# Kernel optimization log

Measured on AMD Instinct MI355X. Metric: run time of the kernel, lower is better.

## Reference

```python
import jax, jax.numpy as jnp
import numpy as np

D_CAT = 4096   # number of multinomial categories (input_dim)
HID = 256      # hidden_dim
B = 4096       # batch_size (eta is a (B, D_CAT-1) parameter)
INIT = 1e-3
LOG2PI = float(np.log(2.0 * np.pi))


def _helmert_basis(d):
    """Orthonormal ILR balance basis, shape (d-1, d): rows sum to 0, Psi @ Psi.T = I."""
    i = np.arange(1, d, dtype=np.float64)
    scale = np.sqrt(i / (i + 1.0))
    Psi = np.zeros((d - 1, d), dtype=np.float64)
    tri = np.tril(np.ones((d - 1, d - 1), dtype=np.float64))
    Psi[:, : d - 1] = tri * (scale / i)[:, None]
    Psi[np.arange(d - 1), np.arange(1, d)] = -scale
    return Psi.astype(np.float32)


def setup_inputs() -> dict:
    key = jax.random.key(0)
    k1, k2, k3, k4 = jax.random.split(key, 4)
    n = D_CAT - 1
    x = jax.random.randint(k1, (B, D_CAT), 0, 20).astype(jnp.float32)  # count data
    Psi = jnp.asarray(_helmert_basis(D_CAT))                            # (n, D)
    enc_W = jax.random.normal(k2, (HID, n), dtype=jnp.float32) * INIT   # encoder Linear weight
    dec_W = jax.random.normal(k3, (n, HID), dtype=jnp.float32) * INIT   # decoder Linear weight
    variational_logvars = jnp.zeros((HID,), jnp.float32)
    log_sigma_sq = jnp.float32(0.01)
    eta = jax.random.normal(k4, (B, n), dtype=jnp.float32) * INIT       # learned eta parameter
    return dict(x=x, Psi=Psi, enc_W=enc_W, dec_W=dec_W,
                variational_logvars=variational_logvars,
                log_sigma_sq=log_sigma_sq, eta=eta)


def reference(x, Psi, enc_W, dec_W, variational_logvars, log_sigma_sq, eta):
    # --- ILR transform of imputed counts: clr(log(x+1)) @ Psi^T ---
    logp = jnp.log(x + 1.0)                                   # imputer: x + 1
    clr = logp - logp.mean(-1, keepdims=True)                 # (B, D)
    hx = clr @ Psi.T                                          # (B, n)
    z_mean = hx @ enc_W.T                                     # (B, k)
    mu = z_mean @ dec_W.T                                     # (B, n)

    # --- MultivariateNormalFactorIdentity log_prob via Woodbury / det lemma ---
    # Sigma = var * I_n + W diag(Dv) W^T,  W = dec_W (n, k)
    Dv = jnp.exp(variational_logvars)                         # (k,)
    var = jnp.exp(log_sigma_sq)                               # scalar
    n = dec_W.shape[0]
    WtW = dec_W.T @ dec_W                                     # (k, k)
    M = jnp.diag(1.0 / Dv) + WtW / var                        # capacitance matrix (k, k)
    d = eta - mu                                              # (B, n)
    dW = d @ dec_W                                            # (B, k)
    sol = jnp.linalg.solve(M, dW.T).T                         # (B, k)
    quad = jnp.sum(d * d, -1) / var - jnp.sum(dW * sol, -1) / (var * var)
    _, logdetM = jnp.linalg.slogdet(M)
    logdet_sigma = n * log_sigma_sq + jnp.sum(variational_logvars) + logdetM
    logit_loss = jnp.mean(-0.5 * (n * LOG2PI + logdet_sigma + quad))

    # --- standard-normal prior on z_mean ---
    prior_loss = jnp.mean(-0.5 * z_mean * z_mean - 0.5 * LOG2PI)

    # --- Multinomial log-likelihood with logits = ilr_inv(eta) = eta @ Psi ---
    logits = eta @ Psi                                        # (B, D)
    logsm = jax.nn.log_softmax(logits, -1)
    ntot = x.sum(-1)
    mult = (jax.lax.lgamma(ntot + 1.0)
            - jnp.sum(jax.lax.lgamma(x + 1.0), -1)
            + jnp.sum(x * logsm, -1))
    mult_loss = jnp.mean(mult)

    return -(mult_loss + logit_loss + prior_loss)
```

## Files before the change

kernel.cpp:

```cpp
#include <hip/hip_runtime.h>
#include <math.h>

static constexpr int DC  = 4096;
static constexpr int NM1 = 4095;
static constexpr int HID = 256;
static constexpr int BB  = 4096;
static constexpr double LOG2PI_D = 1.8378770664093454835;

typedef __attribute__((ext_vector_type(8))) __bf16 bf16x8;
typedef __attribute__((ext_vector_type(4))) __bf16 bf16x4;
typedef __attribute__((ext_vector_type(2))) __bf16 bf16x2;
typedef __attribute__((ext_vector_type(4))) float  f32x4;

__device__ __forceinline__ void async16(const __bf16* g, __bf16* l) {
    __builtin_amdgcn_global_load_lds(
        (const __attribute__((address_space(1))) void*)g,
        (__attribute__((address_space(3))) void*)l, 16, 0, 0);
}

__global__ __launch_bounds__(256) void k_pre(
    const float* __restrict__ decW, const float* __restrict__ Psi,
    const float* __restrict__ lv, const float* __restrict__ lss,
    __bf16* __restrict__ decWT, float* __restrict__ av, float* __restrict__ bv,
    float* __restrict__ Dv, float* __restrict__ scal)
{
    __shared__ float tp[32][33];
    const int t = threadIdx.x;
    const int blk = blockIdx.x;
    if (blk < 1024) {
        int bx = blk & 7, by = blk >> 3;
        int tx = t & 31, ty = t >> 5;
        int r0 = by * 32, c0 = bx * 32;
        #pragma unroll
        for (int i = 0; i < 4; i++) {
            int r = r0 + ty + i * 8, c = c0 + tx;
            tp[ty + i * 8][tx] = (r < NM1 && c < HID) ? decW[(size_t)r * HID + c] : 0.f;
        }
        __syncthreads();
        #pragma unroll
        for (int i = 0; i < 4; i++) {
            int c = c0 + ty + i * 8, r = r0 + tx;
            decWT[(size_t)c * DC + r] = (__bf16)tp[tx][ty + i * 8];
        }
    } else if (blk < 1040) {
        int r = (blk - 1024) * 256 + t;
        if (r < NM1) {
            av[r] = Psi[(size_t)r * DC];
            bv[r] = -Psi[(size_t)r * DC + r + 1];
        } else { av[r] = 0.f; bv[r] = 0.f; }
    } else {
        float v = lv[t];
        Dv[t] = expf(v);
        for (int o = 32; o > 0; o >>= 1) v += __shfl_down(v, o);
        __shared__ float red[4];
        if ((t & 63) == 0) red[t >> 6] = v;
        __syncthreads();
        if (t == 0) {
            scal[0] = expf(lss[0]);
            scal[1] = red[0] + red[1] + red[2] + red[3];
        }
    }
}

__global__ __launch_bounds__(256) void k_mega(
    const float* __restrict__ x, const float* __restrict__ eta,
    const float* __restrict__ encW, const __bf16* __restrict__ decWT,
    const float* __restrict__ av, const float* __restrict__ bv,
    float* __restrict__ multv, float* __restrict__ eta2,
    __bf16* __restrict__ clrB, __bf16* __restrict__ etaB,
    __bf16* __restrict__ encPsiB, float* __restrict__ WtW)
{
    __shared__ float smemf[2392];
    const int t = threadIdx.x;
    const int blk = blockIdx.x;
    const int lane = t & 63, w = t >> 6;

    if (blk >= 64 + HID) {
        __bf16* es    = (__bf16*)smemf;
        float* red    = smemf + 2048;
        float* wsumE  = smemf + 2064;
        float* wsumX  = smemf + 2068;
        float* firstX = smemf + 2072;
        float* lutL   = smemf + 2328;
        float* lutG   = smemf + 2360;
        const int b = blk - (64 + HID);
        const int j0 = t * 16;

        const float4* xrow = (const float4*)(x + (size_t)b * DC + j0);
        float4 xq[4];
        #pragma unroll
        for (int i = 0; i < 4; i++) xq[i] = xrow[i];

        const float* erow = eta + (size_t)b * NM1;
        float ee[16];
        #pragma unroll
        for (int i = 0; i < 16; i++) { int j = i * 256 + t; ee[i] = (j < NM1) ? erow[j] : 0.f; }

        float avc[16], bvc[16];
        #pragma unroll
        for (int i = 0; i < 16; i += 4) {
            float4 a4 = *(const float4*)(av + j0 + i);
            avc[i] = a4.x; avc[i + 1] = a4.y; avc[i + 2] = a4.z; avc[i + 3] = a4.w;
            float4 b4 = *(const float4*)(bv + j0 + i);
            bvc[i] = b4.x; bvc[i + 1] = b4.y; bvc[i + 2] = b4.z; bvc[i + 3] = b4.w;
        }

        if (t < 32) { float f = (float)t + 1.f; lutL[t] = logf(f); lutG[t] = lgammaf(f); }
        __syncthreads();

        float xv[16], lvv[16];
        #pragma unroll
        for (int i = 0; i < 4; i++) {
            xv[i * 4 + 0] = xq[i].x; xv[i * 4 + 1] = xq[i].y;
            xv[i * 4 + 2] = xq[i].z; xv[i * 4 + 3] = xq[i].w;
        }
        float s = 0.f, slg = 0.f, slp = 0.f;
        #pragma unroll
        for (int i = 0; i < 16; i++) {
            float vf = xv[i];
            int iv = (int)vf;
            float l, g;
            if (vf == (float)iv && iv >= 0 && iv < 32) { l = lutL[iv]; g = lutG[iv]; }
            else { l = logf(vf + 1.f); g = lgammaf(vf + 1.f); }
            lvv[i] = l;
            s += vf; slg += g; slp += l;
        }
        float e2 = 0.f;
        #pragma unroll
        for (int i = 0; i < 16; i++) {
            float e = ee[i];
            e2 += e * e;
            es[i * 256 + t] = (__bf16)e;
        }
        firstX[t] = xv[0];
        for (int o = 32; o > 0; o >>= 1) {
            s += __shfl_down(s, o); slg += __shfl_down(slg, o);
            slp += __shfl_down(slp, o); e2 += __shfl_down(e2, o);
        }
        if (lane == 0) { red[w] = s; red[4 + w] = slg; red[8 + w] = slp; red[12 + w] = e2; }
        __syncthreads();

        const float ntotv  = red[0] + red[1] + red[2] + red[3];
        const float sumlgv = red[4] + red[5] + red[6] + red[7];
        const float m = (red[8] + red[9] + red[10] + red[11]) * (1.f / DC);

        bf16x8 e0 = *(const bf16x8*)(es + j0);
        bf16x8 e1 = *(const bf16x8*)(es + j0 + 8);
        *(bf16x8*)(etaB + (size_t)b * DC + j0)     = e0;
        *(bf16x8*)(etaB + (size_t)b * DC + j0 + 8) = e1;
        float ev[16];
        #pragma unroll
        for (int i = 0; i < 8; i++) { ev[i] = (float)e0[i]; ev[i + 8] = (float)e1[i]; }

        bf16x8 c0, c1;
        #pragma unroll
        for (int i = 0; i < 8; i++) {
            c0[i] = (__bf16)(lvv[i] - m);
            c1[i] = (__bf16)(lvv[i + 8] - m);
        }
        *(bf16x8*)(clrB + (size_t)b * DC + j0)     = c0;
        *(bf16x8*)(clrB + (size_t)b * DC + j0 + 8) = c1;

        float localE = 0.f, localX = 0.f;
        #pragma unroll
        for (int i = 0; i < 16; i++) { localE += ev[i] * avc[i]; localX += xv[i]; }
        float incE = localE, incX = localX;
        #pragma unroll
        for (int o = 1; o < 64; o <<= 1) {
            float vE = __shfl_up(incE, o), vX = __shfl_up(incX, o);
            if (lane >= o) { incE += vE; incX += vX; }
        }
        if (lane == 63) { wsumE[w] = incE; wsumX[w] = incX; }
        float eprev = (t > 0) ? (float)es[j0 - 1] : 0.f;
        float bprev = (t > 0) ? bv[j0 - 1] : 0.f;
        float xnl   = (t < 255) ? firstX[t + 1] : 0.f;
        __syncthreads();

        float woffE = 0.f, woffX = 0.f;
        for (int i = 0; i < w; i++) { woffE += wsumE[i]; woffX += wsumX[i]; }
        const float U = wsumE[0] + wsumE[1] + wsumE[2] + wsumE[3];
        float runE = woffE + incE - localE;
        float Xrun = woffX + incX - localX;

        float se = 0.f, sx = 0.f;
        #pragma unroll
        for (int i = 0; i < 16; i++) {
            float Tj = U - runE;
            runE += ev[i] * avc[i];
            float pw = (i == 0) ? eprev * bprev : ev[i - 1] * bvc[i - 1];
            float l = Tj - pw;
            se += expf(l);
            Xrun += xv[i];
            float xn = (i < 15) ? xv[i + 1] : xnl;
            sx += ev[i] * (avc[i] * Xrun - bvc[i] * xn);
        }
        for (int o = 32; o > 0; o >>= 1) {
            se += __shfl_down(se, o); sx += __shfl_down(sx, o);
        }
        if (lane == 0) { red[0 + w] = se; red[4 + w] = sx; }
        __syncthreads();
        if (t == 0) {
            float S1t = red[0] + red[1] + red[2] + red[3];
            float S2t = red[4] + red[5] + red[6] + red[7];
            float e2t = red[12] + red[13] + red[14] + red[15];
            double mult = (double)lgammaf(ntotv + 1.f) - (double)sumlgv
                        + (double)S2t - (double)ntotv * (double)logf(S1t);
            multv[b] = (float)mult;
            eta2[b]  = e2t;
        }
    } else if (blk >= 64) {
        __bf16* es   = (__bf16*)smemf;
        float* wsumE = smemf + 2048;
        const int h = blk - 64;
        const float* erow = encW + (size_t)h * NM1;
        float ee[16];
        #pragma unroll
        for (int i = 0; i < 16; i++) { int j = i * 256 + t; ee[i] = (j < NM1) ? erow[j] : 0.f; }
        const int j0 = t * 16;
        float avc[16], bvc[16];
        #pragma unroll
        for (int i = 0; i < 16; i += 4) {
            float4 a4 = *(const float4*)(av + j0 + i);
            avc[i] = a4.x; avc[i + 1] = a4.y; avc[i + 2] = a4.z; avc[i + 3] = a4.w;
            float4 b4 = *(const float4*)(bv + j0 + i);
            bvc[i] = b4.x; bvc[i + 1] = b4.y; bvc[i + 2] = b4.z; bvc[i + 3] = b4.w;
        }
        #pragma unroll
        for (int i = 0; i < 16; i++) es[i * 256 + t] = (__bf16)ee[i];
        __syncthreads();
        float ev[16];
        {
            bf16x8 ea = *(const bf16x8*)(es + j0), eb8 = *(const bf16x8*)(es + j0 + 8);
            #pragma unroll
            for (int i = 0; i < 8; i++) { ev[i] = (float)ea[i]; ev[i + 8] = (float)eb8[i]; }
        }
        float localE = 0.f;
        #pragma unroll
        for (int i = 0; i < 16; i++) localE += ev[i] * avc[i];
        float incE = localE;
        #pragma unroll
        for (int o = 1; o < 64; o <<= 1) { float vE = __shfl_up(incE, o); if (lane >= o) incE += vE; }
        if (lane == 63) wsumE[w] = incE;
        float eprev = (t > 0) ? (float)es[j0 - 1] : 0.f;
        float bprev = (t > 0) ? bv[j0 - 1] : 0.f;
        __syncthreads();
        float woffE = 0.f;
        for (int i = 0; i < w; i++) woffE += wsumE[i];
        const float U = wsumE[0] + wsumE[1] + wsumE[2] + wsumE[3];
        float runE = woffE + incE - localE;
        bf16x8 o0, o1;
        #pragma unroll
        for (int i = 0; i < 16; i++) {
            float Tj = U - runE;
            runE += ev[i] * avc[i];
            float pw = (i == 0) ? eprev * bprev : ev[i - 1] * bvc[i - 1];
            float l = Tj - pw;
            if (i < 8) o0[i] = (__bf16)l; else o1[i - 8] = (__bf16)l;
        }
        *(bf16x8*)(encPsiB + (size_t)h * DC + j0)     = o0;
        *(bf16x8*)(encPsiB + (size_t)h * DC + j0 + 8) = o1;
    } else {
        __bf16* As = (__bf16*)smemf;
        __bf16* Bs = (__bf16*)(smemf + 1024);
        const int w2 = blk;
        const int mn = w2 & 15, sl = w2 >> 4;
        const int m0 = (mn >> 2) * 64, n0 = (mn & 3) * 64, kb = sl * 1024;
        const int ln = lane & 15, q = lane >> 4;
        const int wm = w >> 1, wn = w & 1;
        f32x4 acc[2][2] = {};
        for (int k0 = kb; k0 < kb + 1024; k0 += 32) {
            async16(decWT + (size_t)(m0 + (t >> 2)) * DC + k0 + (t & 3) * 8, As + t * 8);
            async16(decWT + (size_t)(n0 + (t >> 2)) * DC + k0 + (t & 3) * 8, Bs + t * 8);
            __syncthreads();
            bf16x8 af[2], bfr[2];
            #pragma unroll
            for (int i = 0; i < 2; i++) {
                af[i]  = *(const bf16x8*)(As + (wm * 32 + i * 16 + ln) * 32 + q * 8);
                bfr[i] = *(const bf16x8*)(Bs + (wn * 32 + i * 16 + ln) * 32 + q * 8);
            }
            #pragma unroll
            for (int mi = 0; mi < 2; mi++)
                #pragma unroll
                for (int ni = 0; ni < 2; ni++)
                    acc[mi][ni] = __builtin_amdgcn_mfma_f32_16x16x32_bf16(af[mi], bfr[ni], acc[mi][ni], 0, 0, 0);
            __syncthreads();
        }
        #pragma unroll
        for (int mi = 0; mi < 2; mi++)
            #pragma unroll
            for (int rr = 0; rr < 4; rr++) {
                int m = m0 + wm * 32 + mi * 16 + q * 4 + rr;
                #pragma unroll
                for (int ni = 0; ni < 2; ni++)
                    atomicAdd(&WtW[(size_t)m * HID + n0 + wn * 32 + ni * 16 + ln], acc[mi][ni][rr]);
            }
    }
}

__global__ __launch_bounds__(256) void k_combo2(
    const __bf16* __restrict__ clrB, const __bf16* __restrict__ etaB,
    const __bf16* __restrict__ encPsiB, const __bf16* __restrict__ decWT,
    float* __restrict__ part,
    const float* __restrict__ WtW, const float* __restrict__ Dv,
    const float* __restrict__ scal, __bf16* __restrict__ WtWB,
    __bf16* __restrict__ MinvB, float* __restrict__ scal_out)
{
    __shared__ __bf16 As[64 * 64];
    __shared__ __bf16 Bs[256 * 64];
    const int tid = threadIdx.x;
    const int w = tid >> 6, lane = tid & 63;
    const int ln = lane & 15, q = lane >> 4;
    const int wm = w >> 1, wn = w & 1;
    const int bid = blockIdx.x;

    if (bid >= 16) {
        const int idx = bid - 16;
        const int g = idx >> 8, r = idx & 255, sl = r >> 6, mt = r & 63;
        const __bf16* A  = g ? etaB  : clrB;
        const __bf16* Bt = g ? decWT : encPsiB;
        float* C = part + ((size_t)(g * 4 + sl) << 20);
        const int m0 = mt * 64, kb = sl * 1024;
        f32x4 acc[2][8] = {};
        for (int k0 = kb; k0 < kb + 1024; k0 += 64) {
            #pragma unroll
            for (int j = 0; j < 2; j++) {
                int c = j * 256 + tid;
                int row = c >> 3, ch = c & 7;
                async16(A + (size_t)(m0 + row) * DC + k0 + (ch ^ (row & 7)) * 8, As + c * 8);
            }
            #pragma unroll
            for (int j = 0; j < 8; j++) {
                int c = j * 256 + tid;
                int row = c >> 3, ch = c & 7;
                async16(Bt + (size_t)row * DC + k0 + (ch ^ (row & 7)) * 8, Bs + c * 8);
            }
            __syncthreads();
            #pragma unroll
            for (int jj = 0; jj < 2; jj++) {
                bf16x8 af[2], bfr[8];
                #pragma unroll
                for (int i = 0; i < 2; i++) {
                    int arow = wm * 32 + i * 16 + ln;
                    af[i]  = *(const bf16x8*)(As + arow * 64 + ((jj * 4 + q) ^ (arow & 7)) * 8);
                }
                #pragma unroll
                for (int i = 0; i < 8; i++) {
                    int brow = wn * 128 + i * 16 + ln;
                    bfr[i] = *(const bf16x8*)(Bs + brow * 64 + ((jj * 4 + q) ^ (brow & 7)) * 8);
                }
                #pragma unroll
                for (int mi = 0; mi < 2; mi++)
                    #pragma unroll
                    for (int ni = 0; ni < 8; ni++)
                        acc[mi][ni] = __builtin_amdgcn_mfma_f32_16x16x32_bf16(af[mi], bfr[ni], acc[mi][ni], 0, 0, 0);
            }
            __syncthreads();
        }
        #pragma unroll
        for (int mi = 0; mi < 2; mi++)
            #pragma unroll
            for (int rr = 0; rr < 4; rr++) {
                int m = m0 + wm * 32 + mi * 16 + q * 4 + rr;
                #pragma unroll
                for (int ni = 0; ni < 8; ni++) {
                    int n = wn * 128 + ni * 16 + ln;
                    C[(size_t)m * HID + n] = acc[mi][ni][rr];
                }
            }
    } else {
        __shared__ float dvs[HID];
        __shared__ float redc[8];
        const int w2 = bid;
        const int m0 = (w2 >> 2) * 64, n0 = (w2 & 3) * 64;
        dvs[tid] = Dv[tid];
        __syncthreads();
        const float rv = 1.f / scal[0];
        f32x4 acc[2][2] = {};
        for (int k0 = 0; k0 < HID; k0 += 32) {
            {
                int row = tid >> 2, kc = tid & 3;
                const float* srcA = WtW + (size_t)(m0 + row) * HID + k0 + kc * 8;
                const float* srcB = WtW + (size_t)(n0 + row) * HID + k0 + kc * 8;
                float sA = dvs[m0 + row] * rv;
                bf16x8 a8, b8;
                #pragma unroll
                for (int u = 0; u < 8; u++) {
                    a8[u] = (__bf16)(srcA[u] * sA);
                    b8[u] = (__bf16)(srcB[u] * dvs[k0 + kc * 8 + u] * rv);
                }
                *(bf16x8*)(As + tid * 8) = a8;
                *(bf16x8*)(Bs + tid * 8) = b8;
            }
            __syncthreads();
            bf16x8 af[2], bfr[2];
            #pragma unroll
            for (int i = 0; i < 2; i++) {
                af[i]  = *(const bf16x8*)(As + (wm * 32 + i * 16 + ln) * 32 + q * 8);
                bfr[i] = *(const bf16x8*)(Bs + (wn * 32 + i * 16 + ln) * 32 + q * 8);
            }
            #pragma unroll
            for (int mi = 0; mi < 2; mi++)
                #pragma unroll
                for (int ni = 0; ni < 2; ni++)
                    acc[mi][ni] = __builtin_amdgcn_mfma_f32_16x16x32_bf16(af[mi], bfr[ni], acc[mi][ni], 0, 0, 0);
            __syncthreads();
        }
        float t1p = 0.f, t2p = 0.f;
        #pragma unroll
        for (int mi = 0; mi < 2; mi++)
            #pragma unroll
            for (int rr = 0; rr < 4; rr++) {
                int m = m0 + wm * 32 + mi * 16 + q * 4 + rr;
                #pragma unroll
                for (int ni = 0; ni < 2; ni++) {
                    int n = n0 + wn * 32 + ni * 16 + ln;
                    float wmn = WtW[(size_t)m * HID + n];
                    float Bmn = dvs[m] * wmn * rv;
                    float Bnm = dvs[n] * wmn * rv;
                    float mv = (((m == n) ? 1.f : 0.f) - Bmn + acc[mi][ni][rr]) * dvs[n];
                    MinvB[(size_t)m * HID + n] = (__bf16)mv;
                    WtWB[(size_t)m * HID + n] = (__bf16)wmn;
                    t2p += Bmn * Bnm;
                    if (m == n) t1p += Bmn;
                }
            }
        for (int o = 32; o > 0; o >>= 1) { t1p += __shfl_down(t1p, o); t2p += __shfl_down(t2p, o); }
        if (lane == 0) { redc[w] = t1p; redc[4 + w] = t2p; }
        __syncthreads();
        if (tid == 0) {
            atomicAdd(&scal_out[2], redc[0] + redc[1] + redc[2] + redc[3]);
            atomicAdd(&scal_out[3], redc[4] + redc[5] + redc[6] + redc[7]);
        }
    }
}

__global__ __launch_bounds__(256) void mfma_quad(
    const float* __restrict__ part,
    const __bf16* __restrict__ WtWB, const __bf16* __restrict__ MinvB,
    float* __restrict__ r0a, float* __restrict__ r1a, float* __restrict__ r2a,
    float* __restrict__ r3a)
{
    __shared__ __bf16 As[16 * 32];
    __shared__ __bf16 Bs[256 * 32];
    __shared__ __bf16 dWs[16 * 264];
    const int tid = threadIdx.x;
    const int w = tid >> 6, lane = tid & 63;
    const int ln = lane & 15, q = lane >> 4;
    const int m0 = blockIdx.x * 16;
    const float* zp = part;
    const float* ep = part + ((size_t)4 << 20);
    const size_t SL = (size_t)1 << 20;

    f32x4 acc[4] = {};
    for (int k0 = 0; k0 < HID; k0 += 32) {
        {
            int row = tid >> 4, kc = tid & 15;
            size_t off = (size_t)(m0 + row) * HID + k0 + kc * 2;
            float2 v0 = *(const float2*)(zp + off);
            float2 v1 = *(const float2*)(zp + SL + off);
            float2 v2 = *(const float2*)(zp + 2 * SL + off);
            float2 v3 = *(const float2*)(zp + 3 * SL + off);
            float vx = v0.x + v1.x + v2.x + v3.x;
            float vy = v0.y + v1.y + v2.y + v3.y;
            bf16x2 b2 = {(__bf16)vx, (__bf16)vy};
            int ch = kc >> 2, wi = kc & 3;
            *(bf16x2*)(As + row * 32 + ((ch ^ ((row >> 1) & 3)) * 8) + wi * 2) = b2;
        }
        #pragma unroll
        for (int j = 0; j < 4; j++) {
            int c = j * 256 + tid;
            int row = c >> 2, ch = c & 3;
            async16(WtWB + (size_t)row * HID + k0 + (ch ^ ((row >> 1) & 3)) * 8, Bs + c * 8);
        }
        __syncthreads();
        bf16x8 af = *(const bf16x8*)(As + ln * 32 + ((q ^ ((ln >> 1) & 3)) * 8));
        #pragma unroll
        for (int ni = 0; ni < 4; ni++) {
            int brow = w * 64 + ni * 16 + ln;
            bf16x8 bfr = *(const bf16x8*)(Bs + brow * 32 + ((q ^ ((ln >> 1) & 3)) * 8));
            acc[ni] = __builtin_amdgcn_mfma_f32_16x16x32_bf16(af, bfr, acc[ni], 0, 0, 0);
        }
        __syncthreads();
    }
    #pragma unroll
    for (int rr = 0; rr < 4; rr++) {
        int lm = q * 4 + rr;
        int m = m0 + lm;
        float s0 = 0.f, s1 = 0.f, s3 = 0.f;
        #pragma unroll
        for (int ni = 0; ni < 4; ni++) {
            int n = w * 64 + ni * 16 + ln;
            size_t o2 = (size_t)m * HID + n;
            float zv = zp[o2] + zp[SL + o2] + zp[2 * SL + o2] + zp[3 * SL + o2];
            float ew = ep[o2] + ep[SL + o2] + ep[2 * SL + o2] + ep[3 * SL + o2];
            float dv = ew - acc[ni][rr];
            dWs[lm * 264 + n] = (__bf16)dv;
            s0 += ew * zv; s1 += dv * zv; s3 += zv * zv;
        }
        #pragma unroll
        for (int o = 1; o < 16; o <<= 1) {
            s0 += __shfl_xor(s0, o); s1 += __shfl_xor(s1, o); s3 += __shfl_xor(s3, o);
        }
        if (ln == 0) {
            atomicAdd(&r0a[m], s0); atomicAdd(&r1a[m], s1); atomicAdd(&r3a[m], s3);
        }
    }

    f32x4 acc2[4] = {};
    for (int k0 = 0; k0 < HID; k0 += 32) {
        #pragma unroll
        for (int j = 0; j < 4; j++) {
            int c = j * 256 + tid;
            int row = c >> 2, ch = c & 3;
            async16(MinvB + (size_t)row * HID + k0 + (ch ^ ((row >> 1) & 3)) * 8, Bs + c * 8);
        }
        __syncthreads();
        bf16x8 af = *(const bf16x8*)(dWs + ln * 264 + k0 + q * 8);
        #pragma unroll
        for (int ni = 0; ni < 4; ni++) {
            int brow = w * 64 + ni * 16 + ln;
            bf16x8 bfr = *(const bf16x8*)(Bs + brow * 32 + ((q ^ ((ln >> 1) & 3)) * 8));
            acc2[ni] = __builtin_amdgcn_mfma_f32_16x16x32_bf16(af, bfr, acc2[ni], 0, 0, 0);
        }
        __syncthreads();
    }
    #pragma unroll
    for (int rr = 0; rr < 4; rr++) {
        int lm = q * 4 + rr;
        int m = m0 + lm;
        float s2 = 0.f;
        #pragma unroll
        for (int ni = 0; ni < 4; ni++) {
            int n = w * 64 + ni * 16 + ln;
            s2 += (float)dWs[lm * 264 + n] * acc2[ni][rr];
        }
        #pragma unroll
        for (int o = 1; o < 16; o <<= 1) s2 += __shfl_xor(s2, o);
        if (ln == 0) atomicAdd(&r2a[m], s2);
    }
}

__global__ void k_final(const float* __restrict__ multv, const float* __restrict__ eta2,
                        const float* __restrict__ r0a, const float* __restrict__ r1a,
                        const float* __restrict__ r2a, const float* __restrict__ r3a,
                        const float* __restrict__ scal, const float* __restrict__ lss,
                        float* __restrict__ out) {
    int t = threadIdx.x;
    float var = scal[0];
    float rv = 1.f / var;
    double am = 0.0, aq = 0.0, az = 0.0;
    for (int b = t; b < BB; b += 256) {
        am += (double)multv[b];
        aq += (double)((eta2[b] - r0a[b] - r1a[b]) * rv - r2a[b] * rv * rv);
        az += (double)r3a[b];
    }
    for (int o = 32; o > 0; o >>= 1) {
        am += __shfl_down(am, o); aq += __shfl_down(aq, o); az += __shfl_down(az, o);
    }
    __shared__ double red[3][4];
    if ((t & 63) == 0) { int w = t >> 6; red[0][w] = am; red[1][w] = aq; red[2][w] = az; }
    __syncthreads();
    if (t == 0) {
        double mm = (red[0][0] + red[0][1] + red[0][2] + red[0][3]) / (double)BB;
        double mq = (red[1][0] + red[1][1] + red[1][2] + red[1][3]) / (double)BB;
        double mz = (red[2][0] + red[2][1] + red[2][2] + red[2][3]) / ((double)BB * (double)HID);
        double t1 = scal[2], t2 = scal[3];
        double logdetIB = t1 - t2 * 0.5;
        double sumlv = (double)scal[1];
        double logdetM = -sumlv + logdetIB;
        double logdet_sigma = (double)NM1 * (double)lss[0] + sumlv + logdetM;
        double logit_loss = -0.5 * ((double)NM1 * LOG2PI_D + logdet_sigma + mq);
        double prior_loss = -0.5 * mz - 0.5 * LOG2PI_D;
        out[0] = (float)(-(mm + logit_loss + prior_loss));
    }
}


extern "C" void kernel_launch(void* const* d_in, const int* in_sizes, int n_in,
                              void* d_out, int out_size, void* d_ws, size_t ws_size,
                              hipStream_t stream) {
    (void)in_sizes; (void)n_in; (void)out_size; (void)ws_size;
    const float* x    = (const float*)d_in[0];
    const float* Psi  = (const float*)d_in[1];
    const float* encW = (const float*)d_in[2];
    const float* decW = (const float*)d_in[3];
    const float* lv   = (const float*)d_in[4];
    const float* lss  = (const float*)d_in[5];
    const float* eta  = (const float*)d_in[6];
    float* out = (float*)d_out;

    float* wp = (float*)d_ws;
    float* part   = wp;
    float* WtW    = part + ((size_t)8 << 20);
    float* r0a    = WtW    + 65536;
    float* r1a    = r0a    + 4096;
    float* r2a    = r1a    + 4096;
    float* r3a    = r2a    + 4096;
    float* scal   = r3a    + 4096;
    float* av     = scal   + 16;
    float* bv     = av     + 4096;
    float* multv  = bv     + 4096;
    float* eta2   = multv  + 4096;
    float* Dv     = eta2   + 4096;
    __bf16* clrB    = (__bf16*)(Dv + 256);
    __bf16* etaB    = clrB    + (1 << 24);
    __bf16* encPsiB = etaB    + (1 << 24);
    __bf16* decWT   = encPsiB + (1 << 20);
    __bf16* WtWB    = decWT   + (1 << 20);
    __bf16* MinvB   = WtWB    + 65536;

    hipMemsetAsync(WtW, 0, (size_t)(65536 + 4 * 4096 + 16) * sizeof(float), stream);

    k_pre<<<1041, 256, 0, stream>>>(decW, Psi, lv, lss, decWT, av, bv, Dv, scal);

    k_mega<<<64 + HID + BB, 256, 0, stream>>>(x, eta, encW, decWT, av, bv,
                                              multv, eta2, clrB, etaB, encPsiB, WtW);

    k_combo2<<<528, 256, 0, stream>>>(clrB, etaB, encPsiB, decWT, part,
                                      WtW, Dv, scal, WtWB, MinvB, scal);

    mfma_quad<<<256, 256, 0, stream>>>(part, WtWB, MinvB, r0a, r1a, r2a, r3a);

    k_final<<<1, 256, 0, stream>>>(multv, eta2, r0a, r1a, r2a, r3a, scal, lss, out);
}
```

Baseline: 283.4 us.

## Double-buffer GEMM tiles in k_combo2 and split N across blocks

The split-K GEMM path in k_combo2 now double-buffers its A and B shared-memory tiles, prefetching the next K-slice with async global-to-LDS loads while MFMAs run on the current one, and uses explicit vmcnt waits and barriers. The 256-wide N dimension is split into two 128-wide tiles, which halves per-block accumulators and B traffic and doubles the grid from 528 to 1040 blocks. The intent is to overlap memory latency with compute and raise occupancy. In exchange, each block re-reads its A tile for both N halves, and the hand-written waitcnt sequencing is fragile.

New measurement: 269.8 us. 4.8% less time.

```diff
diff --git a/kernel.cpp b/kernel.cpp
--- a/kernel.cpp
+++ b/kernel.cpp
@@ -305,8 +305,8 @@
     const float* __restrict__ scal, __bf16* __restrict__ WtWB,
     __bf16* __restrict__ MinvB, float* __restrict__ scal_out)
 {
-    __shared__ __bf16 As[64 * 64];
-    __shared__ __bf16 Bs[256 * 64];
+    __shared__ __bf16 AsB[2][64 * 64];
+    __shared__ __bf16 BsB[2][128 * 64];
     const int tid = threadIdx.x;
     const int w = tid >> 6, lane = tid & 63;
     const int ln = lane & 15, q = lane >> 4;
@@ -315,46 +315,69 @@
 
     if (bid >= 16) {
         const int idx = bid - 16;
-        const int g = idx >> 8, r = idx & 255, sl = r >> 6, mt = r & 63;
+        const int g = idx >> 9;
+        const int r = idx & 511;
+        const int sl = r >> 7;
+        const int mt = (r & 127) >> 1;
+        const int nt = r & 1;
         const __bf16* A  = g ? etaB  : clrB;
         const __bf16* Bt = g ? decWT : encPsiB;
         float* C = part + ((size_t)(g * 4 + sl) << 20);
-        const int m0 = mt * 64, kb = sl * 1024;
-        f32x4 acc[2][8] = {};
-        for (int k0 = kb; k0 < kb + 1024; k0 += 64) {
+        const int m0 = mt * 64, n0 = nt * 128, kb = sl * 1024;
+
+        auto stage = [&](int buf, int k0) {
             #pragma unroll
             for (int j = 0; j < 2; j++) {
                 int c = j * 256 + tid;
                 int row = c >> 3, ch = c & 7;
-                async16(A + (size_t)(m0 + row) * DC + k0 + (ch ^ (row & 7)) * 8, As + c * 8);
-            }
-            #pragma unroll
-            for (int j = 0; j < 8; j++) {
+                async16(A + (size_t)(m0 + row) * DC + k0 + (ch ^ (row & 7)) * 8,
+                        &AsB[buf][c * 8]);
+            }
+            #pragma unroll
+            for (int j = 0; j < 4; j++) {
                 int c = j * 256 + tid;
                 int row = c >> 3, ch = c & 7;
-                async16(Bt + (size_t)row * DC + k0 + (ch ^ (row & 7)) * 8, Bs + c * 8);
-            }
-            __syncthreads();
+                async16(Bt + (size_t)(n0 + row) * DC + k0 + (ch ^ (row & 7)) * 8,
+                        &BsB[buf][c * 8]);
+            }
+        };
+
+        f32x4 acc[2][4] = {};
+        stage(0, kb);
+        int cur = 0;
+        for (int t = 0; t < 16; t++) {
+            if (t < 15) {
+                stage(cur ^ 1, kb + (t + 1) * 64);
+                asm volatile("s_waitcnt vmcnt(6)" ::: "memory");
+            } else {
+                asm volatile("s_waitcnt vmcnt(0)" ::: "memory");
+            }
+            __builtin_amdgcn_s_barrier();
+            const __bf16* As = AsB[cur];
+            const __bf16* Bs = BsB[cur];
             #pragma unroll
             for (int jj = 0; jj < 2; jj++) {
-                bf16x8 af[2], bfr[8];
+                bf16x8 af[2], bfr[4];
                 #pragma unroll
                 for (int i = 0; i < 2; i++) {
                     int arow = wm * 32 + i * 16 + ln;
                     af[i]  = *(const bf16x8*)(As + arow * 64 + ((jj * 4 + q) ^ (arow & 7)) * 8);
                 }
                 #pragma unroll
-                for (int i = 0; i < 8; i++) {
-                    int brow = wn * 128 + i * 16 + ln;
+                for (int i = 0; i < 4; i++) {
+                    int brow = wn * 64 + i * 16 + ln;
                     bfr[i] = *(const bf16x8*)(Bs + brow * 64 + ((jj * 4 + q) ^ (brow & 7)) * 8);
                 }
                 #pragma unroll
                 for (int mi = 0; mi < 2; mi++)
                     #pragma unroll
-                    for (int ni = 0; ni < 8; ni++)
+                    for (int ni = 0; ni < 4; ni++)
                         acc[mi][ni] = __builtin_amdgcn_mfma_f32_16x16x32_bf16(af[mi], bfr[ni], acc[mi][ni], 0, 0, 0);
             }
-            __syncthreads();
+            asm volatile("s_waitcnt lgkmcnt(0)" ::: "memory");
+            __builtin_amdgcn_sched_barrier(0);
+            __builtin_amdgcn_s_barrier();
+            cur ^= 1;
         }
         #pragma unroll
         for (int mi = 0; mi < 2; mi++)
@@ -362,14 +385,16 @@
             for (int rr = 0; rr < 4; rr++) {
                 int m = m0 + wm * 32 + mi * 16 + q * 4 + rr;
                 #pragma unroll
-                for (int ni = 0; ni < 8; ni++) {
-                    int n = wn * 128 + ni * 16 + ln;
+                for (int ni = 0; ni < 4; ni++) {
+                    int n = n0 + wn * 64 + ni * 16 + ln;
                     C[(size_t)m * HID + n] = acc[mi][ni][rr];
                 }
             }
     } else {
         __shared__ float dvs[HID];
         __shared__ float redc[8];
+        __bf16* As = AsB[0];
+        __bf16* Bs = BsB[0];
         const int w2 = bid;
         const int m0 = (w2 >> 2) * 64, n0 = (w2 & 3) * 64;
         dvs[tid] = Dv[tid];
@@ -616,8 +641,8 @@
     k_mega<<<64 + HID + BB, 256, 0, stream>>>(x, eta, encW, decWT, av, bv,
                                               multv, eta2, clrB, etaB, encPsiB, WtW);
 
-    k_combo2<<<528, 256, 0, stream>>>(clrB, etaB, encPsiB, decWT, part,
-                                      WtW, Dv, scal, WtWB, MinvB, scal);
+    k_combo2<<<1040, 256, 0, stream>>>(clrB, etaB, encPsiB, decWT, part,
+                                       WtW, Dv, scal, WtWB, MinvB, scal);
 
     mfma_quad<<<256, 256, 0, stream>>>(part, WtWB, MinvB, r0a, r1a, r2a, r3a);
 
```
